# Performance work log

Measured on AMD Instinct MI355X. Metric: run time of the kernel, lower is better.

## Reference

```python
import jax, jax.numpy as jnp
import numpy as np

B, T, C = 2, 4096, 512
H, DH = 8, 64            # num_heads, num_head_channels (per-head dim after reshape)
COND = 512
SCALE = (DH // H) ** -0.5  # faithful to original: (num_head_channels // num_heads)**-0.5


def setup_inputs() -> dict:
    key = jax.random.key(0)
    ks = jax.random.split(key, 6)
    x = jax.random.normal(ks[0], (B, T, C), dtype=jnp.float32)
    condition = jax.random.normal(ks[1], (B, T, COND), dtype=jnp.float32)
    W_qk = jax.random.normal(ks[2], (COND, 2 * H * DH), dtype=jnp.float32) * (COND ** -0.5)
    W_v = jax.random.normal(ks[3], (C, H * DH), dtype=jnp.float32) * (C ** -0.5)
    W_u = jax.random.normal(ks[4], (H * DH, C), dtype=jnp.float32) * ((H * DH) ** -0.5)
    b_u = jax.random.normal(ks[5], (C,), dtype=jnp.float32) * 0.01
    return {"x": x, "condition": condition, "W_qk": W_qk, "W_v": W_v, "W_u": W_u, "b_u": b_u}


def reference(x, condition, W_qk, W_v, W_u, b_u):
    b, t, _ = x.shape
    qk = condition @ W_qk                                  # [b, t, 2*H*DH]
    q, k = jnp.split(qk, 2, axis=-1)
    q = q.reshape(b, t, H, DH).transpose(0, 2, 1, 3)       # [b, H, t, DH]
    k = k.reshape(b, t, H, DH).transpose(0, 2, 1, 3)
    v = (x @ W_v).reshape(b, t, H, DH).transpose(0, 2, 1, 3)
    q = q * SCALE
    dots = jnp.einsum('bhid,bhjd->bhij', q, k)             # [b, H, t, t] (1 GB score matrix)
    attn = jax.nn.softmax(dots, axis=-1)
    out = jnp.einsum('bhij,bhjd->bhid', attn, v)           # [b, H, t, DH]
    out = out.transpose(0, 2, 1, 3).reshape(b, t, H * DH)
    return out @ W_u + b_u
```

## Files before the change

kernel.cpp:

```cpp
#include <hip/hip_runtime.h>

#define B_SZ 2
#define T_SZ 4096

typedef unsigned short u16;
typedef __attribute__((ext_vector_type(8))) short short8;
typedef __attribute__((ext_vector_type(4))) float f32x4;
typedef __attribute__((ext_vector_type(4))) unsigned short u16x4;

#define CEXP 0.51006973f

__device__ __forceinline__ u16 f2bf(float f) {
    unsigned int u;
    __builtin_memcpy(&u, &f, 4);
    u = (u + 0x7fffu + ((u >> 16) & 1u)) >> 16;
    return (u16)u;
}
__device__ __forceinline__ unsigned int rbits(float f) {
    unsigned int u;
    __builtin_memcpy(&u, &f, 4);
    return u + 0x8000u;
}
__device__ __forceinline__ f32x4 mfma16(short8 a, short8 b, f32x4 c) {
    return __builtin_amdgcn_mfma_f32_16x16x32_bf16(a, b, c, 0, 0, 0);
}

__global__ void k_prep(const float* __restrict__ x, const float* __restrict__ cond,
                       const float* __restrict__ Wqk, const float* __restrict__ Wv,
                       const float* __restrict__ Wu, u16* __restrict__ xb, u16* __restrict__ cb,
                       u16* __restrict__ Wqk_t, u16* __restrict__ Wv_t, u16* __restrict__ Wu_t) {
    int blk = blockIdx.x;
    if (blk < 8192) {
        const float* s = blk < 4096 ? x : cond;
        u16* d = blk < 4096 ? xb : cb;
        int i = ((blk & 4095) * 256 + threadIdx.x) * 4;
        float4 v = *(const float4*)(s + i);
        u16x4 o = { f2bf(v.x), f2bf(v.y), f2bf(v.z), f2bf(v.w) };
        *(u16x4*)(d + i) = o;
    } else if (blk < 10240) {
        int idx = (blk - 8192) * 256 + threadIdx.x;
        Wqk_t[(size_t)(idx & 1023) * 512 + (idx >> 10)] = f2bf(Wqk[idx]);
    } else if (blk < 11264) {
        int idx = (blk - 10240) * 256 + threadIdx.x;
        Wv_t[(size_t)(idx & 511) * 512 + (idx >> 9)] = f2bf(Wv[idx]);
    } else {
        int idx = (blk - 11264) * 256 + threadIdx.x;
        Wu_t[(size_t)(idx & 511) * 512 + (idx >> 9)] = f2bf(Wu[idx]);
    }
}

template <typename OutT, int MODE, int TM, int TN>
__global__ __launch_bounds__(256) void k_gemm5(const u16* __restrict__ A, const u16* __restrict__ Bt,
                                               const float* __restrict__ bias, OutT* __restrict__ C,
                                               OutT* __restrict__ C2) {
    const int K = 512;
    constexpr int MI = TM / 32, NJ = TN / 32;
    constexpr int NA = TM / 64, NB = TN / 64;
    int m0 = blockIdx.x * TM, n0 = blockIdx.y * TN;
    int tid = threadIdx.x;
    int wave = tid >> 6, lane = tid & 63, l16 = lane & 15, q = lane >> 4;
    int mo = (wave & 1) * (TM / 2), no = (wave >> 1) * (TN / 2);

    __shared__ __align__(16) u16 As[TM * 72];
    __shared__ __align__(16) u16 Bs[TN * 72];

    f32x4 acc[MI][NJ];
#pragma unroll
    for (int i = 0; i < MI; ++i)
#pragma unroll
        for (int j = 0; j < NJ; ++j) acc[i][j] = (f32x4){0.f, 0.f, 0.f, 0.f};

    const u16* ap[NA]; const u16* bp[NB];
    short8 ra[NA], rb[NB];
#pragma unroll
    for (int jj = 0; jj < NA; ++jj) {
        int id = tid + 256 * jj;
        ap[jj] = A + (size_t)(m0 + (id >> 2)) * K + (id & 3) * 8;
        ra[jj] = *(const short8*)(ap[jj]);
    }
#pragma unroll
    for (int jj = 0; jj < NB; ++jj) {
        int id = tid + 256 * jj;
        bp[jj] = Bt + (size_t)(n0 + (id >> 2)) * K + (id & 3) * 8;
        rb[jj] = *(const short8*)(bp[jj]);
    }

#pragma unroll 1
    for (int k0 = 0; k0 < K; k0 += 32) {
        __syncthreads();
#pragma unroll
        for (int jj = 0; jj < NA; ++jj) {
            int id = tid + 256 * jj;
            *(short8*)(&As[(id >> 2) * 72 + (id & 3) * 8]) = ra[jj];
        }
#pragma unroll
        for (int jj = 0; jj < NB; ++jj) {
            int id = tid + 256 * jj;
            *(short8*)(&Bs[(id >> 2) * 72 + (id & 3) * 8]) = rb[jj];
        }
        __syncthreads();

        int kadv = (k0 + 32 < K) ? 32 : 0;
#pragma unroll
        for (int jj = 0; jj < NA; ++jj) { ap[jj] += kadv; ra[jj] = *(const short8*)(ap[jj]); }
#pragma unroll
        for (int jj = 0; jj < NB; ++jj) { bp[jj] += kadv; rb[jj] = *(const short8*)(bp[jj]); }
        __builtin_amdgcn_sched_barrier(0);

        short8 af[MI], bf[NJ];
#pragma unroll
        for (int i = 0; i < MI; ++i) af[i] = *(const short8*)(&As[(mo + i * 16 + l16) * 72 + q * 8]);
#pragma unroll
        for (int j = 0; j < NJ; ++j) bf[j] = *(const short8*)(&Bs[(no + j * 16 + l16) * 72 + q * 8]);
#pragma unroll
        for (int i = 0; i < MI; ++i)
#pragma unroll
            for (int j = 0; j < NJ; ++j) acc[i][j] = mfma16(af[i], bf[j], acc[i][j]);
    }

#pragma unroll
    for (int i = 0; i < MI; ++i) {
        int mb = m0 + mo + i * 16 + q * 4;
#pragma unroll
        for (int j = 0; j < NJ; ++j) {
            int nc = n0 + no + j * 16 + l16;
            if constexpr (MODE == 0) {
                float4 bb = *(const float4*)(bias + mb);
                float4 w = { acc[i][j][0] + bb.x, acc[i][j][1] + bb.y,
                             acc[i][j][2] + bb.z, acc[i][j][3] + bb.w };
                *(float4*)(&C[(size_t)nc * 512 + mb]) = w;
            } else if constexpr (MODE == 1) {
                int b = nc >> 12, t = nc & 4095;
                int h = (mb & 511) >> 6, d = mb & 63;
                size_t addr = ((size_t)((b * 8 + h) * 4096 + t)) * 64 + d;
                if (mb < 512) {
                    u16x4 w = { f2bf(acc[i][j][0] * CEXP), f2bf(acc[i][j][1] * CEXP),
                                f2bf(acc[i][j][2] * CEXP), f2bf(acc[i][j][3] * CEXP) };
                    *(u16x4*)(&C[addr]) = w;
                } else {
                    u16x4 w = { f2bf(acc[i][j][0]), f2bf(acc[i][j][1]),
                                f2bf(acc[i][j][2]), f2bf(acc[i][j][3]) };
                    *(u16x4*)(&C2[addr]) = w;
                }
            } else {
                int b = mb >> 12, t = mb & 4095;
                int kt = t >> 6, k64 = t & 63;
                int h = nc >> 6, d = nc & 63;
                size_t addr = ((((size_t)(b * 8 + h) * 64 + kt) * 64 + d) << 6) + k64;
                u16x4 w = { f2bf(acc[i][j][0]), f2bf(acc[i][j][1]),
                            f2bf(acc[i][j][2]), f2bf(acc[i][j][3]) };
                *(u16x4*)(&C[addr]) = w;
            }
        }
    }
}

__global__ __launch_bounds__(512) void k_flash(const u16* __restrict__ Qh, const u16* __restrict__ Kh,
                                               const u16* __restrict__ Vb, u16* __restrict__ o) {
    int bid = blockIdx.x;
    int h = bid & 7, qt = (bid >> 3) & 31, b = bid >> 8;
    int tid = threadIdx.x;
    int wave = tid >> 6, lane = tid & 63, l16 = lane & 15, q = lane >> 4;
    int ks = wave >> 2, w4 = wave & 3;
    int t256 = tid & 255;

    __shared__ __align__(16) u16 smem[2 * (64 * 80 + 64 * 72)];
    u16* Kt = smem + ks * (64 * 80 + 64 * 72);
    u16* Vt = Kt + 64 * 80;

    int head = b * 8 + h;
    short8 qf[2][2];
#pragma unroll
    for (int g = 0; g < 2; ++g) {
        const u16* qp = Qh + ((size_t)head * 4096 + qt * 128 + g * 64 + w4 * 16 + l16) * 64 + q * 8;
        qf[g][0] = *(const short8*)(qp);
        qf[g][1] = *(const short8*)(qp + 32);
    }

    const u16* kb = Kh + (size_t)head * 4096 * 64;
    const u16* vb = Vb + (size_t)head * 4096 * 64;

    int r0 = t256 >> 3, g0 = t256 & 7;
    u16* kw0 = &Kt[r0 * 80 + g0 * 8];
    u16* kw1 = &Kt[(r0 + 32) * 80 + g0 * 8];
    u16* vw0 = &Vt[r0 * 72 + g0 * 8];
    u16* vw1 = &Vt[(r0 + 32) * 72 + g0 * 8];

    f32x4 oacc[2][4];
#pragma unroll
    for (int g = 0; g < 2; ++g)
#pragma unroll
        for (int c = 0; c < 4; ++c) oacc[g][c] = (f32x4){0.f, 0.f, 0.f, 0.f};
    f32x4 lacc[2];
    lacc[0] = (f32x4){0.f, 0.f, 0.f, 0.f};
    lacc[1] = (f32x4){0.f, 0.f, 0.f, 0.f};
    const short8 ones = { 0x3F80, 0x3F80, 0x3F80, 0x3F80, 0x3F80, 0x3F80, 0x3F80, 0x3F80 };
    int pi0 = (l16 >> 2) * 8 + (l16 & 3);

    size_t off0 = (size_t)(ks * 32 + (qt & 31)) * 4096;
    short8 rk0 = *(const short8*)(kb + off0 + t256 * 8);
    short8 rk1 = *(const short8*)(kb + off0 + t256 * 8 + 2048);
    short8 rv0 = *(const short8*)(vb + off0 + t256 * 8);
    short8 rv1 = *(const short8*)(vb + off0 + t256 * 8 + 2048);

#pragma unroll 1
    for (int it = 0; it < 32; ++it) {
        __syncthreads();
        *(short8*)kw0 = rk0;
        *(short8*)kw1 = rk1;
        *(short8*)vw0 = rv0;
        *(short8*)vw1 = rv1;
        __syncthreads();

        size_t offn = (size_t)(ks * 32 + ((qt + it + 1) & 31)) * 4096;
        rk0 = *(const short8*)(kb + offn + t256 * 8);
        rk1 = *(const short8*)(kb + offn + t256 * 8 + 2048);
        rv0 = *(const short8*)(vb + offn + t256 * 8);
        rv1 = *(const short8*)(vb + offn + t256 * 8 + 2048);
        __builtin_amdgcn_sched_barrier(0);

#pragma unroll
        for (int kk = 0; kk < 2; ++kk) {
            const u16* ka = &Kt[(kk * 32 + pi0) * 80 + q * 8];
            short8 A00 = *(const short8*)(ka);
            short8 A01 = *(const short8*)(ka + 32);
            short8 A10 = *(const short8*)(ka + 4 * 80);
            short8 A11 = *(const short8*)(ka + 4 * 80 + 32);
            short8 vfc[4];
#pragma unroll
            for (int c = 0; c < 4; ++c)
                vfc[c] = *(const short8*)(&Vt[(c * 16 + l16) * 72 + kk * 32 + q * 8]);

#pragma unroll
            for (int g = 0; g < 2; ++g) {
                f32x4 s0 = (f32x4){0.f, 0.f, 0.f, 0.f};
                f32x4 s1 = (f32x4){0.f, 0.f, 0.f, 0.f};
                s0 = mfma16(A00, qf[g][0], s0); s0 = mfma16(A01, qf[g][1], s0);
                s1 = mfma16(A10, qf[g][0], s1); s1 = mfma16(A11, qf[g][1], s1);

                uint4 pd;
                pd.x = __builtin_amdgcn_perm(rbits(__builtin_amdgcn_exp2f(s0[1])),
                                             rbits(__builtin_amdgcn_exp2f(s0[0])), 0x07060302u);
                pd.y = __builtin_amdgcn_perm(rbits(__builtin_amdgcn_exp2f(s0[3])),
                                             rbits(__builtin_amdgcn_exp2f(s0[2])), 0x07060302u);
                pd.z = __builtin_amdgcn_perm(rbits(__builtin_amdgcn_exp2f(s1[1])),
                                             rbits(__builtin_amdgcn_exp2f(s1[0])), 0x07060302u);
                pd.w = __builtin_amdgcn_perm(rbits(__builtin_amdgcn_exp2f(s1[3])),
                                             rbits(__builtin_amdgcn_exp2f(s1[2])), 0x07060302u);
                short8 pf;
                __builtin_memcpy(&pf, &pd, 16);

                lacc[g] = mfma16(ones, pf, lacc[g]);
#pragma unroll
                for (int c = 0; c < 4; ++c)
                    oacc[g][c] = mfma16(vfc[c], pf, oacc[g][c]);
            }
        }
    }

    __syncthreads();
    float* red = (float*)smem;
    if (ks == 1) {
        float* rp = red + ((w4 * 64 + lane) * 37);
#pragma unroll
        for (int g = 0; g < 2; ++g)
#pragma unroll
            for (int c = 0; c < 4; ++c)
#pragma unroll
                for (int r = 0; r < 4; ++r) rp[g * 16 + c * 4 + r] = oacc[g][c][r];
        rp[32] = lacc[0][0];
        rp[33] = lacc[1][0];
    }
    __syncthreads();
    if (ks == 0) {
        const float* rp = red + ((w4 * 64 + lane) * 37);
#pragma unroll
        for (int g = 0; g < 2; ++g) {
#pragma unroll
            for (int c = 0; c < 4; ++c)
#pragma unroll
                for (int r = 0; r < 4; ++r) oacc[g][c][r] += rp[g * 16 + c * 4 + r];
            float inv = 1.f / (lacc[g][0] + rp[32 + g]);
            u16* ob = o + (size_t)(b * T_SZ + qt * 128 + g * 64 + w4 * 16 + l16) * 512 + h * 64 + q * 4;
#pragma unroll
            for (int c = 0; c < 4; ++c) {
                u16x4 w = { f2bf(oacc[g][c][0] * inv), f2bf(oacc[g][c][1] * inv),
                            f2bf(oacc[g][c][2] * inv), f2bf(oacc[g][c][3] * inv) };
                *(u16x4*)(ob + c * 16) = w;
            }
        }
    }
}

extern "C" void kernel_launch(void* const* d_in, const int* in_sizes, int n_in,
                              void* d_out, int out_size, void* d_ws, size_t ws_size,
                              hipStream_t stream) {
    const float* x    = (const float*)d_in[0];
    const float* cond = (const float*)d_in[1];
    const float* Wqk  = (const float*)d_in[2];
    const float* Wv   = (const float*)d_in[3];
    const float* Wu   = (const float*)d_in[4];
    const float* bu   = (const float*)d_in[5];
    float* out = (float*)d_out;

    const size_t MT = (size_t)B_SZ * T_SZ;
    u16* xb    = (u16*)d_ws;
    u16* cb    = xb + MT * 512;
    u16* qh_ws = cb + MT * 512;
    u16* kh_ws = qh_ws + MT * 512;
    u16* vb_ws = kh_ws + MT * 512;
    u16* at_ws = vb_ws + MT * 512;
    u16* Wqk_t = at_ws + MT * 512;
    u16* Wv_t  = Wqk_t + (size_t)1024 * 512;
    u16* Wu_t  = Wv_t + (size_t)512 * 512;

    k_prep<<<12288, 256, 0, stream>>>(x, cond, Wqk, Wv, Wu, xb, cb, Wqk_t, Wv_t, Wu_t);

    k_gemm5<u16, 1, 128, 64><<<dim3(8, 128), 256, 0, stream>>>(Wqk_t, cb, nullptr, qh_ws, kh_ws);
    k_gemm5<u16, 2, 64, 64><<<dim3(128, 8), 256, 0, stream>>>(xb, Wv_t, nullptr, vb_ws, nullptr);
    k_flash<<<512, 512, 0, stream>>>(qh_ws, kh_ws, vb_ws, at_ws);
    k_gemm5<float, 0, 64, 64><<<dim3(8, 128), 256, 0, stream>>>(Wu_t, at_ws, bu, out, nullptr);
}
```

Measured before the change: 221.9 us.

## Tile weight transposes through shared memory and deepen GEMM global prefetch

The weight transpose in the prep kernel now stages 64x64 tiles in shared memory, so both the fp32 reads and the bf16 writes are coalesced and vectorized. This replaces per-element scattered stores and cuts the launch from 12288 blocks to 8448. The GEMM kernel keeps four K-steps of global loads in flight in registers instead of one, to hide global memory latency better. The cost is more register pressure, which may reduce occupancy.

```diff
diff --git a/kernel.cpp b/kernel.cpp
--- a/kernel.cpp
+++ b/kernel.cpp
@@ -29,23 +29,37 @@
                        const float* __restrict__ Wqk, const float* __restrict__ Wv,
                        const float* __restrict__ Wu, u16* __restrict__ xb, u16* __restrict__ cb,
                        u16* __restrict__ Wqk_t, u16* __restrict__ Wv_t, u16* __restrict__ Wu_t) {
-    int blk = blockIdx.x;
+    int blk = blockIdx.x, tid = threadIdx.x;
     if (blk < 8192) {
         const float* s = blk < 4096 ? x : cond;
         u16* d = blk < 4096 ? xb : cb;
-        int i = ((blk & 4095) * 256 + threadIdx.x) * 4;
+        int i = ((blk & 4095) * 256 + tid) * 4;
         float4 v = *(const float4*)(s + i);
         u16x4 o = { f2bf(v.x), f2bf(v.y), f2bf(v.z), f2bf(v.w) };
         *(u16x4*)(d + i) = o;
-    } else if (blk < 10240) {
-        int idx = (blk - 8192) * 256 + threadIdx.x;
-        Wqk_t[(size_t)(idx & 1023) * 512 + (idx >> 10)] = f2bf(Wqk[idx]);
-    } else if (blk < 11264) {
-        int idx = (blk - 10240) * 256 + threadIdx.x;
-        Wv_t[(size_t)(idx & 511) * 512 + (idx >> 9)] = f2bf(Wv[idx]);
-    } else {
-        int idx = (blk - 11264) * 256 + threadIdx.x;
-        Wu_t[(size_t)(idx & 511) * 512 + (idx >> 9)] = f2bf(Wu[idx]);
+        return;
+    }
+    __shared__ u16 T[64][72];
+    const float* src; u16* dst; int N, ti;
+    if (blk < 8320)      { src = Wqk; dst = Wqk_t; N = 1024; ti = blk - 8192; }
+    else if (blk < 8384) { src = Wv;  dst = Wv_t;  N = 512;  ti = blk - 8320; }
+    else                 { src = Wu;  dst = Wu_t;  N = 512;  ti = blk - 8384; }
+    int nt = N >> 6;
+    int bi = ti / nt, bj = ti - bi * nt;
+    int kb = bi * 64, nb = bj * 64;
+    int r = tid >> 2, c4 = (tid & 3) * 16;
+#pragma unroll
+    for (int jj = 0; jj < 4; ++jj) {
+        float4 v = *(const float4*)(src + (size_t)(kb + r) * N + nb + c4 + jj * 4);
+        u16x4 w = { f2bf(v.x), f2bf(v.y), f2bf(v.z), f2bf(v.w) };
+        *(u16x4*)(&T[r][c4 + jj * 4]) = w;
+    }
+    __syncthreads();
+#pragma unroll
+    for (int jj = 0; jj < 4; ++jj) {
+        int c = c4 + jj * 4;
+        u16x4 w = { T[c][r], T[c + 1][r], T[c + 2][r], T[c + 3][r] };
+        *(u16x4*)(dst + (size_t)(nb + r) * 512 + kb + c) = w;
     }
 }
 
@@ -71,51 +85,60 @@
         for (int j = 0; j < NJ; ++j) acc[i][j] = (f32x4){0.f, 0.f, 0.f, 0.f};
 
     const u16* ap[NA]; const u16* bp[NB];
-    short8 ra[NA], rb[NB];
+    short8 ra[4][NA], rb[4][NB];
 #pragma unroll
     for (int jj = 0; jj < NA; ++jj) {
         int id = tid + 256 * jj;
         ap[jj] = A + (size_t)(m0 + (id >> 2)) * K + (id & 3) * 8;
-        ra[jj] = *(const short8*)(ap[jj]);
     }
 #pragma unroll
     for (int jj = 0; jj < NB; ++jj) {
         int id = tid + 256 * jj;
         bp[jj] = Bt + (size_t)(n0 + (id >> 2)) * K + (id & 3) * 8;
-        rb[jj] = *(const short8*)(bp[jj]);
+    }
+#pragma unroll
+    for (int d = 0; d < 4; ++d) {
+#pragma unroll
+        for (int jj = 0; jj < NA; ++jj) ra[d][jj] = *(const short8*)(ap[jj] + d * 32);
+#pragma unroll
+        for (int jj = 0; jj < NB; ++jj) rb[d][jj] = *(const short8*)(bp[jj] + d * 32);
     }
 
 #pragma unroll 1
-    for (int k0 = 0; k0 < K; k0 += 32) {
-        __syncthreads();
-#pragma unroll
-        for (int jj = 0; jj < NA; ++jj) {
-            int id = tid + 256 * jj;
-            *(short8*)(&As[(id >> 2) * 72 + (id & 3) * 8]) = ra[jj];
+    for (int ko = 0; ko < 4; ++ko) {
+#pragma unroll
+        for (int d = 0; d < 4; ++d) {
+            __syncthreads();
+#pragma unroll
+            for (int jj = 0; jj < NA; ++jj) {
+                int id = tid + 256 * jj;
+                *(short8*)(&As[(id >> 2) * 72 + (id & 3) * 8]) = ra[d][jj];
+            }
+#pragma unroll
+            for (int jj = 0; jj < NB; ++jj) {
+                int id = tid + 256 * jj;
+                *(short8*)(&Bs[(id >> 2) * 72 + (id & 3) * 8]) = rb[d][jj];
+            }
+            __syncthreads();
+
+            int s4 = ko * 4 + d + 4;
+            if (s4 > 15) s4 = 15;
+#pragma unroll
+            for (int jj = 0; jj < NA; ++jj) ra[d][jj] = *(const short8*)(ap[jj] + s4 * 32);
+#pragma unroll
+            for (int jj = 0; jj < NB; ++jj) rb[d][jj] = *(const short8*)(bp[jj] + s4 * 32);
+            __builtin_amdgcn_sched_barrier(0);
+
+            short8 af[MI], bf[NJ];
+#pragma unroll
+            for (int i = 0; i < MI; ++i) af[i] = *(const short8*)(&As[(mo + i * 16 + l16) * 72 + q * 8]);
+#pragma unroll
+            for (int j = 0; j < NJ; ++j) bf[j] = *(const short8*)(&Bs[(no + j * 16 + l16) * 72 + q * 8]);
+#pragma unroll
+            for (int i = 0; i < MI; ++i)
+#pragma unroll
+                for (int j = 0; j < NJ; ++j) acc[i][j] = mfma16(af[i], bf[j], acc[i][j]);
         }
-#pragma unroll
-        for (int jj = 0; jj < NB; ++jj) {
-            int id = tid + 256 * jj;
-            *(short8*)(&Bs[(id >> 2) * 72 + (id & 3) * 8]) = rb[jj];
-        }
-        __syncthreads();
-
-        int kadv = (k0 + 32 < K) ? 32 : 0;
-#pragma unroll
-        for (int jj = 0; jj < NA; ++jj) { ap[jj] += kadv; ra[jj] = *(const short8*)(ap[jj]); }
-#pragma unroll
-        for (int jj = 0; jj < NB; ++jj) { bp[jj] += kadv; rb[jj] = *(const short8*)(bp[jj]); }
-        __builtin_amdgcn_sched_barrier(0);
-
-        short8 af[MI], bf[NJ];
-#pragma unroll
-        for (int i = 0; i < MI; ++i) af[i] = *(const short8*)(&As[(mo + i * 16 + l16) * 72 + q * 8]);
-#pragma unroll
-        for (int j = 0; j < NJ; ++j) bf[j] = *(const short8*)(&Bs[(no + j * 16 + l16) * 72 + q * 8]);
-#pragma unroll
-        for (int i = 0; i < MI; ++i)
-#pragma unroll
-            for (int j = 0; j < NJ; ++j) acc[i][j] = mfma16(af[i], bf[j], acc[i][j]);
     }
 
 #pragma unroll
@@ -314,7 +337,7 @@
     u16* Wv_t  = Wqk_t + (size_t)1024 * 512;
     u16* Wu_t  = Wv_t + (size_t)512 * 512;
 
-    k_prep<<<12288, 256, 0, stream>>>(x, cond, Wqk, Wv, Wu, xb, cb, Wqk_t, Wv_t, Wu_t);
+    k_prep<<<8448, 256, 0, stream>>>(x, cond, Wqk, Wv, Wu, xb, cb, Wqk_t, Wv_t, Wu_t);
 
     k_gemm5<u16, 1, 128, 64><<<dim3(8, 128), 256, 0, stream>>>(Wqk_t, cb, nullptr, qh_ws, kh_ws);
     k_gemm5<u16, 2, 64, 64><<<dim3(128, 8), 256, 0, stream>>>(xb, Wv_t, nullptr, vb_ws, nullptr);
```

Measured after the change: 223.8 us. No clear change (+0.9%).
